# Optimization experiments

Measured on AMD Instinct MI355X. Metric: run time of the kernel, lower is better.

The kernel has to match this reference:

```python
import jax, jax.numpy as jnp
import numpy as np

D = 192          # d_model = d_perc = d_tech
H = 3            # n_heads
HD = D // H      # head_dim = 64
FP = 128         # fingerprint_dim
EPS_LN = 1e-5


def _layernorm(x, g, b):
    mu = jnp.mean(x, axis=-1, keepdims=True)
    var = jnp.var(x, axis=-1, keepdims=True)
    return (x - mu) * jax.lax.rsqrt(var + EPS_LN) * g + b


def setup_inputs() -> dict:
    key = jax.random.key(0)
    ks = jax.random.split(key, 32)
    B = 65536
    s = 0.05
    inp = {
        'perc_vec': jax.random.normal(ks[0], (B, D), jnp.float32),
        'tech_vec': jax.random.normal(ks[1], (B, D), jnp.float32),
        # proj_p / proj_t (torch Linear: [out, in])
        'Wp': jax.random.normal(ks[2], (D, D), jnp.float32) * s,
        'bp': jax.random.normal(ks[3], (D,), jnp.float32) * s,
        'Wt': jax.random.normal(ks[4], (D, D), jnp.float32) * s,
        'bt': jax.random.normal(ks[5], (D,), jnp.float32) * s,
        # MultiheadAttention packed in-proj [3D, D] and out-proj [D, D]
        'in_w': jax.random.normal(ks[6], (3 * D, D), jnp.float32) * s,
        'in_b': jax.random.normal(ks[7], (3 * D,), jnp.float32) * s,
        'out_w': jax.random.normal(ks[8], (D, D), jnp.float32) * s,
        'out_b': jax.random.normal(ks[9], (D,), jnp.float32) * s,
        # FFN
        'ffn_w1': jax.random.normal(ks[10], (2 * D, D), jnp.float32) * s,
        'ffn_b1': jax.random.normal(ks[11], (2 * D,), jnp.float32) * s,
        'ffn_w2': jax.random.normal(ks[12], (D, 2 * D), jnp.float32) * s,
        'ffn_b2': jax.random.normal(ks[13], (D,), jnp.float32) * s,
        # LayerNorms
        'ln1_g': jnp.ones((D,), jnp.float32),
        'ln1_b': jnp.zeros((D,), jnp.float32),
        'ln2_g': jnp.ones((D,), jnp.float32),
        'ln2_b': jnp.zeros((D,), jnp.float32),
        # classifier head
        'cls_w1': jax.random.normal(ks[14], (D, D), jnp.float32) * s,
        'cls_b1': jax.random.normal(ks[15], (D,), jnp.float32) * s,
        'cls_w2': jax.random.normal(ks[16], (3, D), jnp.float32) * s,
        'cls_b2': jax.random.normal(ks[17], (3,), jnp.float32) * s,
        # fingerprint head
        'fp_w': jax.random.normal(ks[18], (FP, D), jnp.float32) * s,
        'fp_b': jax.random.normal(ks[19], (FP,), jnp.float32) * s,
    }
    return inp


def reference(perc_vec, tech_vec, Wp, bp, Wt, bt, in_w, in_b, out_w, out_b,
              ffn_w1, ffn_b1, ffn_w2, ffn_b2, ln1_g, ln1_b, ln2_g, ln2_b,
              cls_w1, cls_b1, cls_w2, cls_b2, fp_w, fp_b):
    B = perc_vec.shape[0]
    # projections -> 2-token sequence [B, 2, D]
    p = perc_vec @ Wp.T + bp
    t = tech_vec @ Wt.T + bt
    seq = jnp.stack([p, t], axis=1)

    # self-attention (eval mode, no dropout)
    qkv = seq @ in_w.T + in_b                     # [B, 2, 3D]
    q, k, v = jnp.split(qkv, 3, axis=-1)
    q = q.reshape(B, 2, H, HD).transpose(0, 2, 1, 3)  # [B, H, 2, HD]
    k = k.reshape(B, 2, H, HD).transpose(0, 2, 1, 3)
    v = v.reshape(B, 2, H, HD).transpose(0, 2, 1, 3)
    scores = jnp.einsum('bhqd,bhkd->bhqk', q, k) / np.sqrt(HD).astype(np.float32)
    attn = jax.nn.softmax(scores, axis=-1)
    ctx = jnp.einsum('bhqk,bhkd->bhqd', attn, v)      # [B, H, 2, HD]
    ctx = ctx.transpose(0, 2, 1, 3).reshape(B, 2, D)
    attn_out = ctx @ out_w.T + out_b

    x = _layernorm(seq + attn_out, ln1_g, ln1_b)
    h = jax.nn.relu(x @ ffn_w1.T + ffn_b1)
    ffn = h @ ffn_w2.T + ffn_b2
    x = _layernorm(x + ffn, ln2_g, ln2_b)

    z = x.mean(axis=1)                                # [B, D]
    logits = jax.nn.relu(z @ cls_w1.T + cls_b1) @ cls_w2.T + cls_b2  # [B, 3]
    probs = jax.nn.sigmoid(logits)
    fp = z @ fp_w.T + fp_b
    fp = fp / jnp.maximum(jnp.linalg.norm(fp, axis=-1, keepdims=True), 1e-12)
    # (presence_p, decode_reliability, artifact_risk, fingerprint)
    return probs[:, 0:1], probs[:, 1:2], probs[:, 2:3], fp
```

## Files before the change

### kernel.cpp

```cpp
#include <hip/hip_runtime.h>
#include <hip/hip_bf16.h>
#include <math.h>

#define D 192
#define RPB 16
typedef unsigned short u16;
typedef __attribute__((ext_vector_type(8))) short short8;
typedef __attribute__((ext_vector_type(4))) float float4v;

__device__ __forceinline__ float b2f(u16 u){ union{unsigned i; float f;}c; c.i=(unsigned)u<<16; return c.f; }
__device__ __forceinline__ u16  f2b(float f){
    union{float f; unsigned i;}c; c.f=f;
    unsigned r = c.i + 0x7FFFu + ((c.i>>16)&1u);
    return (u16)(r>>16);
}
__device__ __forceinline__ float sel4(float a0,float a1,float a2,float a3,int s){
    return s==0?a0:(s==1?a1:(s==2?a2:a3));
}

#define WP_OFF   0
#define WT_OFF   36864
#define INW_OFF  73728
#define OUTW_OFF 184320
#define FW1_OFF  221184
#define FW2_OFF  294912
#define CW1_OFF  368640
#define FPW_OFF  405504
#define W_TOTAL  430080

__global__ __launch_bounds__(256)
void cvt_weights(const float* __restrict__ Wp, const float* __restrict__ Wt,
                 const float* __restrict__ in_w, const float* __restrict__ out_w,
                 const float* __restrict__ fw1, const float* __restrict__ fw2,
                 const float* __restrict__ cw1, const float* __restrict__ fpw,
                 u16* __restrict__ ws)
{
    int idx = blockIdx.x * 256 + threadIdx.x;
    if (idx >= W_TOTAL) return;
    const float* src; int off; int K = 192;
    if      (idx < WT_OFF)   { src = Wp;   off = WP_OFF; }
    else if (idx < INW_OFF)  { src = Wt;   off = WT_OFF; }
    else if (idx < OUTW_OFF) { src = in_w; off = INW_OFF; }
    else if (idx < FW1_OFF)  { src = out_w;off = OUTW_OFF; }
    else if (idx < FW2_OFF)  { src = fw1;  off = FW1_OFF; }
    else if (idx < CW1_OFF)  { src = fw2;  off = FW2_OFF; K = 384; }
    else if (idx < FPW_OFF)  { src = cw1;  off = CW1_OFF; }
    else                     { src = fpw;  off = FPW_OFF; }
    int lin = idx - off;
    int n = lin / K, k = lin - n*K;
    int swz = ((n>>4)*(K>>5) + (k>>5))*512 + ((n&15)<<5) + (k&31);
    ws[off + swz] = f2b(src[lin]);
}

template<int KT, int MT>
__device__ __forceinline__ void load_afrags(short8 (&A)[MT][KT], const u16* base,
                                            int stride, int lane16, int quad)
{
    #pragma unroll
    for (int mt = 0; mt < MT; ++mt)
        #pragma unroll
        for (int ks = 0; ks < KT; ++ks)
            A[mt][ks] = *(const short8*)(base + (mt*16 + lane16)*stride + ks*32 + quad*8);
}

template<int KT, int MT, int NTW>
__device__ __forceinline__ void run_gemm(const short8 (&A)[MT][KT],
    const u16* __restrict__ wsb, const float* __restrict__ bias,
    u16* dst, float* dstf, int dstride,
    const u16* resid, int rstride, bool relu, int rmul, int roff,
    int wave, int lane16, int quad)
{
    #pragma unroll
    for (int i = 0; i < NTW; ++i) {
        int nt = wave + 4*i, n0 = nt*16;
        float4v c[MT];
        #pragma unroll
        for (int mt = 0; mt < MT; ++mt) c[mt] = (float4v){0.f,0.f,0.f,0.f};
        #pragma unroll
        for (int ks = 0; ks < KT; ++ks) {
            short8 b = *(const short8*)(wsb + (size_t)((nt*KT + ks)<<9) + (lane16<<5) + (quad<<3));
            #pragma unroll
            for (int mt = 0; mt < MT; ++mt)
                c[mt] = __builtin_amdgcn_mfma_f32_16x16x32_bf16(A[mt][ks], b, c[mt], 0,0,0);
        }
        float bv = bias[n0 + lane16];
        #pragma unroll
        for (int mt = 0; mt < MT; ++mt)
            #pragma unroll
            for (int ii = 0; ii < 4; ++ii) {
                int dr = (mt*16 + quad*4 + ii)*rmul + roff;
                float v = c[mt][ii] + bv;
                if (resid) v += b2f(resid[dr*rstride + n0 + lane16]);
                if (relu)  v = fmaxf(v, 0.f);
                if (dst) dst [dr*dstride + n0 + lane16] = f2b(v);
                else     dstf[dr*dstride + n0 + lane16] = v;
            }
    }
}

#define S1 200
#define SH 392
#define A_INP 0
#define A_INT 3200
#define A_SEQ 6400
#define A_CTX 0
#define A_X1  6400
#define A_H   0
#define A_Z   0
#define A_CH  3200
#define A_FPF 6400
#define ARENA_U16 12800

__global__ __launch_bounds__(256, 4)
void fusion_mfma_kernel(
    const float* __restrict__ perc, const float* __restrict__ tech,
    const float* __restrict__ bp,   const float* __restrict__ bt,
    const float* __restrict__ in_b, const float* __restrict__ out_b,
    const float* __restrict__ fb1,  const float* __restrict__ fb2,
    const float* __restrict__ ln1g, const float* __restrict__ ln1b,
    const float* __restrict__ ln2g, const float* __restrict__ ln2b,
    const float* __restrict__ cb1,  const float* __restrict__ cw2,
    const float* __restrict__ cb2,  const float* __restrict__ fpb,
    const u16*   __restrict__ ws,
    float* __restrict__ out, int B)
{
    __shared__ __align__(16) u16 arena[ARENA_U16];
    __shared__ __align__(16) float satt[16][3][4];
    __shared__ float wavered[4][32][2];
    __shared__ float smu[32], srs[32], srn[16];

    const int tid = threadIdx.x;
    const int wave = tid >> 6, lane = tid & 63;
    const int lane16 = lane & 15, quad = lane >> 4;
    const int row0 = blockIdx.x * RPB;
    float* fpf = (float*)(arena + A_FPF);

    #pragma unroll
    for (int it = 0; it < 3; ++it) {
        int idx = it*256 + tid;
        int arr = idx >= 384 ? 1 : 0;
        int rem = arr ? idx - 384 : idx;
        int r = rem / 24, g = rem - r*24;
        const float* src = arr ? tech : perc;
        const float4* s4 = (const float4*)(src + (size_t)(row0 + r)*D + g*8);
        float4 lo = s4[0], hi = s4[1];
        short8 o;
        o[0]=(short)f2b(lo.x); o[1]=(short)f2b(lo.y); o[2]=(short)f2b(lo.z); o[3]=(short)f2b(lo.w);
        o[4]=(short)f2b(hi.x); o[5]=(short)f2b(hi.y); o[6]=(short)f2b(hi.z); o[7]=(short)f2b(hi.w);
        *(short8*)(arena + (arr ? A_INT : A_INP) + r*S1 + g*8) = o;
    }
    __syncthreads();

    {
        short8 A1[1][6];
        load_afrags<6,1>(A1, arena + A_INP, S1, lane16, quad);
        run_gemm<6,1,3>(A1, ws + WP_OFF, bp, arena + A_SEQ, nullptr, S1,
                        nullptr, 0, false, 2, 0, wave, lane16, quad);
        load_afrags<6,1>(A1, arena + A_INT, S1, lane16, quad);
        run_gemm<6,1,3>(A1, ws + WT_OFF, bt, arena + A_SEQ, nullptr, S1,
                        nullptr, 0, false, 2, 1, wave, lane16, quad);
    }
    __syncthreads();

    short8 A2[2][6];
    load_afrags<6,2>(A2, arena + A_SEQ, S1, lane16, quad);
    {
        float* satt_w = (float*)arena;
        #pragma unroll
        for (int i = 0; i < 3; ++i) {
            int nt = wave + 4*i;
            float4v ck[2] = {(float4v){0,0,0,0},(float4v){0,0,0,0}};
            #pragma unroll
            for (int ks = 0; ks < 6; ++ks) {
                short8 b = *(const short8*)(ws + INW_OFF + 192*192 + ((nt*6+ks)<<9) + (lane16<<5) + (quad<<3));
                ck[0] = __builtin_amdgcn_mfma_f32_16x16x32_bf16(A2[0][ks], b, ck[0], 0,0,0);
                ck[1] = __builtin_amdgcn_mfma_f32_16x16x32_bf16(A2[1][ks], b, ck[1], 0,0,0);
            }
            float bvk = in_b[192 + nt*16 + lane16];
            float4v cq[2] = {(float4v){0,0,0,0},(float4v){0,0,0,0}};
            #pragma unroll
            for (int ks = 0; ks < 6; ++ks) {
                short8 b = *(const short8*)(ws + INW_OFF + ((nt*6+ks)<<9) + (lane16<<5) + (quad<<3));
                cq[0] = __builtin_amdgcn_mfma_f32_16x16x32_bf16(A2[0][ks], b, cq[0], 0,0,0);
                cq[1] = __builtin_amdgcn_mfma_f32_16x16x32_bf16(A2[1][ks], b, cq[1], 0,0,0);
            }
            float bvq = in_b[nt*16 + lane16];
            float sc[2][2][4];
            #pragma unroll
            for (int mt = 0; mt < 2; ++mt)
                #pragma unroll
                for (int p = 0; p < 2; ++p) {
                    float q0 = cq[mt][2*p] + bvq, q1 = cq[mt][2*p+1] + bvq;
                    float k0 = ck[mt][2*p] + bvk, k1 = ck[mt][2*p+1] + bvk;
                    sc[mt][p][0] = q0*k0; sc[mt][p][1] = q0*k1;
                    sc[mt][p][2] = q1*k0; sc[mt][p][3] = q1*k1;
                }
            #pragma unroll
            for (int mt = 0; mt < 2; ++mt)
                #pragma unroll
                for (int p = 0; p < 2; ++p)
                    #pragma unroll
                    for (int c = 0; c < 4; ++c) {
                        float v = sc[mt][p][c];
                        v += __shfl_xor(v, 1); v += __shfl_xor(v, 2);
                        v += __shfl_xor(v, 4); v += __shfl_xor(v, 8);
                        sc[mt][p][c] = v;
                    }
            if ((lane16 >> 2) == i) {
                int c = lane16 & 3;
                #pragma unroll
                for (int mt = 0; mt < 2; ++mt)
                    #pragma unroll
                    for (int p = 0; p < 2; ++p) {
                        float vv = sel4(sc[mt][p][0], sc[mt][p][1], sc[mt][p][2], sc[mt][p][3], c);
                        satt_w[(wave*16 + (2*quad + p + 8*mt))*12 + i*4 + c] = vv;
                    }
            }
        }
    }
    __syncthreads();

    if (tid < 96) {
        const float* satt_w = (const float*)arena;
        int r = tid / 6, rem = tid - r*6;
        int h = rem >> 1, qt = rem & 1;
        float s0 = 0.f, s1 = 0.f;
        #pragma unroll
        for (int w = 0; w < 4; ++w) {
            s0 += satt_w[(w*16 + r)*12 + h*4 + qt*2 + 0];
            s1 += satt_w[(w*16 + r)*12 + h*4 + qt*2 + 1];
        }
        s0 *= 0.125f; s1 *= 0.125f;
        float m = fmaxf(s0, s1);
        float e0 = expf(s0 - m), e1 = expf(s1 - m);
        float inv = 1.f / (e0 + e1);
        satt[r][h][qt*2 + 0] = e0 * inv;
        satt[r][h][qt*2 + 1] = e1 * inv;
    }
    __syncthreads();

    #pragma unroll
    for (int i = 0; i < 3; ++i) {
        int nt = wave + 4*i, col = nt*16 + lane16;
        float4v cv[2] = {(float4v){0,0,0,0},(float4v){0,0,0,0}};
        #pragma unroll
        for (int ks = 0; ks < 6; ++ks) {
            short8 b = *(const short8*)(ws + INW_OFF + 384*192 + ((nt*6+ks)<<9) + (lane16<<5) + (quad<<3));
            cv[0] = __builtin_amdgcn_mfma_f32_16x16x32_bf16(A2[0][ks], b, cv[0], 0,0,0);
            cv[1] = __builtin_amdgcn_mfma_f32_16x16x32_bf16(A2[1][ks], b, cv[1], 0,0,0);
        }
        float bv = in_b[384 + col];
        #pragma unroll
        for (int mt = 0; mt < 2; ++mt)
            #pragma unroll
            for (int p = 0; p < 2; ++p) {
                float v0 = cv[mt][2*p] + bv, v1 = cv[mt][2*p+1] + bv;
                int r = 2*quad + p + 8*mt;
                float4 pa = *(const float4*)&satt[r][i][0];
                arena[A_CTX + (2*r    )*S1 + col] = f2b(pa.x*v0 + pa.y*v1);
                arena[A_CTX + (2*r + 1)*S1 + col] = f2b(pa.z*v0 + pa.w*v1);
            }
    }
    __syncthreads();

    float4v x1r[3][2];
    {
        short8 Ac[2][6];
        load_afrags<6,2>(Ac, arena + A_CTX, S1, lane16, quad);
        #pragma unroll
        for (int i = 0; i < 3; ++i) {
            int nt = wave + 4*i, col = nt*16 + lane16;
            x1r[i][0] = (float4v){0,0,0,0}; x1r[i][1] = (float4v){0,0,0,0};
            #pragma unroll
            for (int ks = 0; ks < 6; ++ks) {
                short8 b = *(const short8*)(ws + OUTW_OFF + ((nt*6+ks)<<9) + (lane16<<5) + (quad<<3));
                x1r[i][0] = __builtin_amdgcn_mfma_f32_16x16x32_bf16(Ac[0][ks], b, x1r[i][0], 0,0,0);
                x1r[i][1] = __builtin_amdgcn_mfma_f32_16x16x32_bf16(Ac[1][ks], b, x1r[i][1], 0,0,0);
            }
            float bv = out_b[col];
            #pragma unroll
            for (int mt = 0; mt < 2; ++mt)
                #pragma unroll
                for (int ii = 0; ii < 4; ++ii) {
                    int row = quad*4 + ii + 16*mt;
                    x1r[i][mt][ii] += bv + b2f(arena[A_SEQ + row*S1 + col]);
                }
        }
        float sr[2][4], s2r[2][4];
        #pragma unroll
        for (int mt = 0; mt < 2; ++mt)
            #pragma unroll
            for (int ii = 0; ii < 4; ++ii) {
                float a0 = x1r[0][mt][ii], a1 = x1r[1][mt][ii], a2 = x1r[2][mt][ii];
                float s = a0 + a1 + a2;
                float s2 = a0*a0 + a1*a1 + a2*a2;
                s  += __shfl_xor(s, 1);  s  += __shfl_xor(s, 2);
                s  += __shfl_xor(s, 4);  s  += __shfl_xor(s, 8);
                s2 += __shfl_xor(s2, 1); s2 += __shfl_xor(s2, 2);
                s2 += __shfl_xor(s2, 4); s2 += __shfl_xor(s2, 8);
                sr[mt][ii] = s; s2r[mt][ii] = s2;
            }
        int l = lane16;
        float rowlo = sel4(sr[0][0], sr[0][1], sr[0][2], sr[0][3], l & 3);
        float rowhi = sel4(sr[1][0], sr[1][1], sr[1][2], sr[1][3], l & 3);
        float row2lo = sel4(s2r[0][0], s2r[0][1], s2r[0][2], s2r[0][3], l & 3);
        float row2hi = sel4(s2r[1][0], s2r[1][1], s2r[1][2], s2r[1][3], l & 3);
        float sv = (l & 4) ? rowhi : rowlo;
        float s2v = (l & 4) ? row2hi : row2lo;
        float val = (l & 8) ? s2v : sv;
        wavered[wave][quad*4 + (l & 3) + 16*((l >> 2) & 1)][l >> 3] = val;
    }
    __syncthreads();
    if (tid < 32) {
        float s = 0.f, s2 = 0.f;
        #pragma unroll
        for (int w = 0; w < 4; ++w) { s += wavered[w][tid][0]; s2 += wavered[w][tid][1]; }
        float mu = s * (1.f/192.f);
        float var = s2 * (1.f/192.f) - mu*mu;
        smu[tid] = mu; srs[tid] = rsqrtf(var + 1e-5f);
    }
    __syncthreads();

    #pragma unroll
    for (int i = 0; i < 3; ++i) {
        int col = (wave + 4*i)*16 + lane16;
        float g = ln1g[col], bb = ln1b[col];
        #pragma unroll
        for (int mt = 0; mt < 2; ++mt)
            #pragma unroll
            for (int ii = 0; ii < 4; ++ii) {
                int row = quad*4 + ii + 16*mt;
                float x = (x1r[i][mt][ii] - smu[row]) * srs[row] * g + bb;
                x1r[i][mt][ii] = x;
                arena[A_X1 + row*S1 + col] = f2b(x);
            }
    }
    __syncthreads();

    {
        short8 Ax[2][6];
        load_afrags<6,2>(Ax, arena + A_X1, S1, lane16, quad);
        __syncthreads();
        run_gemm<6,2,6>(Ax, ws + FW1_OFF, fb1, arena + A_H, nullptr, SH,
                        nullptr, 0, true, 1, 0, wave, lane16, quad);
    }
    __syncthreads();

    {
        float4v c2[3][2];
        #pragma unroll
        for (int i = 0; i < 3; ++i) { c2[i][0] = (float4v){0,0,0,0}; c2[i][1] = (float4v){0,0,0,0}; }
        #pragma unroll
        for (int kc = 0; kc < 2; ++kc) {
            short8 Af[2][6];
            load_afrags<6,2>(Af, arena + A_H + kc*192, SH, lane16, quad);
            #pragma unroll
            for (int i = 0; i < 3; ++i) {
                int nt = wave + 4*i;
                #pragma unroll
                for (int ks = 0; ks < 6; ++ks) {
                    short8 b = *(const short8*)(ws + FW2_OFF + ((nt*12 + kc*6 + ks)<<9) + (lane16<<5) + (quad<<3));
                    c2[i][0] = __builtin_amdgcn_mfma_f32_16x16x32_bf16(Af[0][ks], b, c2[i][0], 0,0,0);
                    c2[i][1] = __builtin_amdgcn_mfma_f32_16x16x32_bf16(Af[1][ks], b, c2[i][1], 0,0,0);
                }
            }
        }
        #pragma unroll
        for (int i = 0; i < 3; ++i) {
            float bv = fb2[(wave + 4*i)*16 + lane16];
            #pragma unroll
            for (int mt = 0; mt < 2; ++mt)
                #pragma unroll
                for (int ii = 0; ii < 4; ++ii)
                    c2[i][mt][ii] += bv + x1r[i][mt][ii];
        }
        float sr[2][4], s2r[2][4];
        #pragma unroll
        for (int mt = 0; mt < 2; ++mt)
            #pragma unroll
            for (int ii = 0; ii < 4; ++ii) {
                float a0 = c2[0][mt][ii], a1 = c2[1][mt][ii], a2 = c2[2][mt][ii];
                float s = a0 + a1 + a2;
                float s2 = a0*a0 + a1*a1 + a2*a2;
                s  += __shfl_xor(s, 1);  s  += __shfl_xor(s, 2);
                s  += __shfl_xor(s, 4);  s  += __shfl_xor(s, 8);
                s2 += __shfl_xor(s2, 1); s2 += __shfl_xor(s2, 2);
                s2 += __shfl_xor(s2, 4); s2 += __shfl_xor(s2, 8);
                sr[mt][ii] = s; s2r[mt][ii] = s2;
            }
        int l = lane16;
        float rowlo = sel4(sr[0][0], sr[0][1], sr[0][2], sr[0][3], l & 3);
        float rowhi = sel4(sr[1][0], sr[1][1], sr[1][2], sr[1][3], l & 3);
        float row2lo = sel4(s2r[0][0], s2r[0][1], s2r[0][2], s2r[0][3], l & 3);
        float row2hi = sel4(s2r[1][0], s2r[1][1], s2r[1][2], s2r[1][3], l & 3);
        float sv = (l & 4) ? rowhi : rowlo;
        float s2v = (l & 4) ? row2hi : row2lo;
        float val = (l & 8) ? s2v : sv;
        wavered[wave][quad*4 + (l & 3) + 16*((l >> 2) & 1)][l >> 3] = val;
        __syncthreads();
        if (tid < 32) {
            float s = 0.f, s2 = 0.f;
            #pragma unroll
            for (int w = 0; w < 4; ++w) { s += wavered[w][tid][0]; s2 += wavered[w][tid][1]; }
            float mu = s * (1.f/192.f);
            float var = s2 * (1.f/192.f) - mu*mu;
            smu[tid] = mu; srs[tid] = rsqrtf(var + 1e-5f);
        }
        __syncthreads();
        #pragma unroll
        for (int i = 0; i < 3; ++i) {
            int col = (wave + 4*i)*16 + lane16;
            float g = ln2g[col], bb = ln2b[col];
            #pragma unroll
            for (int mt = 0; mt < 2; ++mt)
                #pragma unroll
                for (int p = 0; p < 2; ++p) {
                    int r = 2*quad + p + 8*mt;
                    float n0v = (c2[i][mt][2*p]   - smu[2*r  ]) * srs[2*r  ] * g + bb;
                    float n1v = (c2[i][mt][2*p+1] - smu[2*r+1]) * srs[2*r+1] * g + bb;
                    arena[A_Z + r*S1 + col] = f2b(0.5f*(n0v + n1v));
                }
        }
    }
    __syncthreads();

    {
        short8 A1[1][6];
        load_afrags<6,1>(A1, arena + A_Z, S1, lane16, quad);
        run_gemm<6,1,3>(A1, ws + CW1_OFF, cb1, arena + A_CH, nullptr, S1,
                        nullptr, 0, true, 1, 0, wave, lane16, quad);
        run_gemm<6,1,2>(A1, ws + FPW_OFF, fpb, nullptr, fpf, 128,
                        nullptr, 0, false, 1, 0, wave, lane16, quad);
    }
    __syncthreads();

    if (tid < 192) {
        int g4 = tid >> 2, sub = tid & 3;
        int r = g4 / 3, cc = g4 - r*3;
        const float* w = cw2 + (size_t)cc * D + sub*48;
        const u16* hr = arena + A_CH + r*S1 + sub*48;
        float a = 0.f;
        #pragma unroll
        for (int i = 0; i < 6; ++i) {
            short8 hv = *(const short8*)(hr + i*8);
            float4 w0 = ((const float4*)w)[2*i], w1 = ((const float4*)w)[2*i+1];
            float wv[8] = {w0.x,w0.y,w0.z,w0.w,w1.x,w1.y,w1.z,w1.w};
            #pragma unroll
            for (int j = 0; j < 8; ++j) a += wv[j] * b2f((u16)hv[j]);
        }
        a += __shfl_xor(a, 1); a += __shfl_xor(a, 2);
        if (sub == 0) {
            a += cb2[cc];
            out[(size_t)cc * B + (size_t)(row0 + r)] = 1.f / (1.f + expf(-a));
        }
    } else {
        int t = tid - 192;
        int r = t >> 2, sub = t & 3;
        const float4* fp4 = (const float4*)(fpf + r*128 + sub*32);
        float s2 = 0.f;
        #pragma unroll
        for (int i = 0; i < 8; ++i) {
            float4 v = fp4[i];
            s2 += v.x*v.x + v.y*v.y + v.z*v.z + v.w*v.w;
        }
        s2 += __shfl_xor(s2, 1); s2 += __shfl_xor(s2, 2);
        if (sub == 0) srn[r] = 1.f / fmaxf(sqrtf(s2), 1e-12f);
    }
    __syncthreads();

    #pragma unroll
    for (int it = 0; it < 2; ++it) {
        int idx = it*256 + tid;
        int r = idx >> 5, c = idx & 31;
        float4 v = ((const float4*)(fpf + r*128))[c];
        float sc = srn[r];
        float4 o; o.x = v.x*sc; o.y = v.y*sc; o.z = v.z*sc; o.w = v.w*sc;
        ((float4*)(out + (size_t)3*B + (size_t)(row0 + r)*128))[c] = o;
    }
}

extern "C" void kernel_launch(void* const* d_in, const int* in_sizes, int n_in,
                              void* d_out, int out_size, void* d_ws, size_t ws_size,
                              hipStream_t stream) {
    if (ws_size < (size_t)W_TOTAL * 2) return;

    const float* perc = (const float*)d_in[0];
    const float* tech = (const float*)d_in[1];
    const float* Wp   = (const float*)d_in[2];
    const float* bp   = (const float*)d_in[3];
    const float* Wt   = (const float*)d_in[4];
    const float* bt   = (const float*)d_in[5];
    const float* in_w = (const float*)d_in[6];
    const float* in_b = (const float*)d_in[7];
    const float* ow   = (const float*)d_in[8];
    const float* ob   = (const float*)d_in[9];
    const float* fw1  = (const float*)d_in[10];
    const float* fb1  = (const float*)d_in[11];
    const float* fw2  = (const float*)d_in[12];
    const float* fb2  = (const float*)d_in[13];
    const float* ln1g = (const float*)d_in[14];
    const float* ln1b = (const float*)d_in[15];
    const float* ln2g = (const float*)d_in[16];
    const float* ln2b = (const float*)d_in[17];
    const float* cw1  = (const float*)d_in[18];
    const float* cb1  = (const float*)d_in[19];
    const float* cw2  = (const float*)d_in[20];
    const float* cb2  = (const float*)d_in[21];
    const float* fpw  = (const float*)d_in[22];
    const float* fpb  = (const float*)d_in[23];

    u16* ws = (u16*)d_ws;
    int B = in_sizes[0] / D;

    hipLaunchKernelGGL(cvt_weights, dim3((W_TOTAL + 255)/256), dim3(256), 0, stream,
                       Wp, Wt, in_w, ow, fw1, fw2, cw1, fpw, ws);

    hipLaunchKernelGGL(fusion_mfma_kernel, dim3(B / RPB), dim3(256), 0, stream,
                       perc, tech, bp, bt, in_b, ob, fb1, fb2,
                       ln1g, ln1b, ln2g, ln2b, cb1, cw2, cb2, fpb,
                       ws, (float*)d_out, B);
}
```

Baseline: 421.7 us.

## Keep LN1 output in LDS instead of registers across FFN to cut VGPRs

The post-attention residual is now written to LDS as bf16 while its row sums are accumulated on the fly, and LayerNorm1 runs as a vectorized in-place pass over LDS. The FFN2 residual is read back from LDS, so the 24-float x1r array no longer stays live across the FFN GEMMs. This lowers register pressure and drops one barrier. In exchange the arena grows (ARENA_U16 from 12800 to 18944), which adds LDS traffic and could limit occupancy. The residual is also rounded to bf16 before LN2, which costs some precision.

```diff
diff --git a/kernel.cpp b/kernel.cpp
--- a/kernel.cpp
+++ b/kernel.cpp
@@ -100,16 +100,16 @@
 
 #define S1 200
 #define SH 392
-#define A_INP 0
-#define A_INT 3200
-#define A_SEQ 6400
+#define A_STG_P 0
+#define A_STG_T 3200
+#define A_SEQ 12544
 #define A_CTX 0
-#define A_X1  6400
+#define A_X1  12544
 #define A_H   0
 #define A_Z   0
 #define A_CH  3200
 #define A_FPF 6400
-#define ARENA_U16 12800
+#define ARENA_U16 18944
 
 __global__ __launch_bounds__(256, 4)
 void fusion_mfma_kernel(
@@ -147,16 +147,16 @@
         short8 o;
         o[0]=(short)f2b(lo.x); o[1]=(short)f2b(lo.y); o[2]=(short)f2b(lo.z); o[3]=(short)f2b(lo.w);
         o[4]=(short)f2b(hi.x); o[5]=(short)f2b(hi.y); o[6]=(short)f2b(hi.z); o[7]=(short)f2b(hi.w);
-        *(short8*)(arena + (arr ? A_INT : A_INP) + r*S1 + g*8) = o;
+        *(short8*)(arena + (arr ? A_STG_T : A_STG_P) + r*S1 + g*8) = o;
     }
     __syncthreads();
 
     {
         short8 A1[1][6];
-        load_afrags<6,1>(A1, arena + A_INP, S1, lane16, quad);
+        load_afrags<6,1>(A1, arena + A_STG_P, S1, lane16, quad);
         run_gemm<6,1,3>(A1, ws + WP_OFF, bp, arena + A_SEQ, nullptr, S1,
                         nullptr, 0, false, 2, 0, wave, lane16, quad);
-        load_afrags<6,1>(A1, arena + A_INT, S1, lane16, quad);
+        load_afrags<6,1>(A1, arena + A_STG_T, S1, lane16, quad);
         run_gemm<6,1,3>(A1, ws + WT_OFF, bt, arena + A_SEQ, nullptr, S1,
                         nullptr, 0, false, 2, 1, wave, lane16, quad);
     }
@@ -263,19 +263,23 @@
     }
     __syncthreads();
 
-    float4v x1r[3][2];
     {
         short8 Ac[2][6];
         load_afrags<6,2>(Ac, arena + A_CTX, S1, lane16, quad);
+        float sa[2][4], s2a[2][4];
+        #pragma unroll
+        for (int mt = 0; mt < 2; ++mt)
+            #pragma unroll
+            for (int ii = 0; ii < 4; ++ii) { sa[mt][ii] = 0.f; s2a[mt][ii] = 0.f; }
         #pragma unroll
         for (int i = 0; i < 3; ++i) {
             int nt = wave + 4*i, col = nt*16 + lane16;
-            x1r[i][0] = (float4v){0,0,0,0}; x1r[i][1] = (float4v){0,0,0,0};
+            float4v c[2] = {(float4v){0,0,0,0},(float4v){0,0,0,0}};
             #pragma unroll
             for (int ks = 0; ks < 6; ++ks) {
                 short8 b = *(const short8*)(ws + OUTW_OFF + ((nt*6+ks)<<9) + (lane16<<5) + (quad<<3));
-                x1r[i][0] = __builtin_amdgcn_mfma_f32_16x16x32_bf16(Ac[0][ks], b, x1r[i][0], 0,0,0);
-                x1r[i][1] = __builtin_amdgcn_mfma_f32_16x16x32_bf16(Ac[1][ks], b, x1r[i][1], 0,0,0);
+                c[0] = __builtin_amdgcn_mfma_f32_16x16x32_bf16(Ac[0][ks], b, c[0], 0,0,0);
+                c[1] = __builtin_amdgcn_mfma_f32_16x16x32_bf16(Ac[1][ks], b, c[1], 0,0,0);
             }
             float bv = out_b[col];
             #pragma unroll
@@ -283,28 +287,27 @@
                 #pragma unroll
                 for (int ii = 0; ii < 4; ++ii) {
                     int row = quad*4 + ii + 16*mt;
-                    x1r[i][mt][ii] += bv + b2f(arena[A_SEQ + row*S1 + col]);
+                    float v = c[mt][ii] + bv + b2f(arena[A_SEQ + row*S1 + col]);
+                    arena[A_X1 + row*S1 + col] = f2b(v);
+                    sa[mt][ii] += v; s2a[mt][ii] += v*v;
                 }
         }
-        float sr[2][4], s2r[2][4];
         #pragma unroll
         for (int mt = 0; mt < 2; ++mt)
             #pragma unroll
             for (int ii = 0; ii < 4; ++ii) {
-                float a0 = x1r[0][mt][ii], a1 = x1r[1][mt][ii], a2 = x1r[2][mt][ii];
-                float s = a0 + a1 + a2;
-                float s2 = a0*a0 + a1*a1 + a2*a2;
+                float s = sa[mt][ii], s2 = s2a[mt][ii];
                 s  += __shfl_xor(s, 1);  s  += __shfl_xor(s, 2);
                 s  += __shfl_xor(s, 4);  s  += __shfl_xor(s, 8);
                 s2 += __shfl_xor(s2, 1); s2 += __shfl_xor(s2, 2);
                 s2 += __shfl_xor(s2, 4); s2 += __shfl_xor(s2, 8);
-                sr[mt][ii] = s; s2r[mt][ii] = s2;
+                sa[mt][ii] = s; s2a[mt][ii] = s2;
             }
         int l = lane16;
-        float rowlo = sel4(sr[0][0], sr[0][1], sr[0][2], sr[0][3], l & 3);
-        float rowhi = sel4(sr[1][0], sr[1][1], sr[1][2], sr[1][3], l & 3);
-        float row2lo = sel4(s2r[0][0], s2r[0][1], s2r[0][2], s2r[0][3], l & 3);
-        float row2hi = sel4(s2r[1][0], s2r[1][1], s2r[1][2], s2r[1][3], l & 3);
+        float rowlo = sel4(sa[0][0], sa[0][1], sa[0][2], sa[0][3], l & 3);
+        float rowhi = sel4(sa[1][0], sa[1][1], sa[1][2], sa[1][3], l & 3);
+        float row2lo = sel4(s2a[0][0], s2a[0][1], s2a[0][2], s2a[0][3], l & 3);
+        float row2hi = sel4(s2a[1][0], s2a[1][1], s2a[1][2], s2a[1][3], l & 3);
         float sv = (l & 4) ? rowhi : rowlo;
         float s2v = (l & 4) ? row2hi : row2lo;
         float val = (l & 8) ? s2v : sv;
@@ -322,25 +325,27 @@
     __syncthreads();
 
     #pragma unroll
-    for (int i = 0; i < 3; ++i) {
-        int col = (wave + 4*i)*16 + lane16;
-        float g = ln1g[col], bb = ln1b[col];
-        #pragma unroll
-        for (int mt = 0; mt < 2; ++mt)
-            #pragma unroll
-            for (int ii = 0; ii < 4; ++ii) {
-                int row = quad*4 + ii + 16*mt;
-                float x = (x1r[i][mt][ii] - smu[row]) * srs[row] * g + bb;
-                x1r[i][mt][ii] = x;
-                arena[A_X1 + row*S1 + col] = f2b(x);
-            }
+    for (int it = 0; it < 3; ++it) {
+        int idx = it*256 + tid;
+        int tok = idx / 24, g = idx - tok*24;
+        float mu = smu[tok], rs = srs[tok];
+        float4 ga = ((const float4*)(ln1g + g*8))[0], gb = ((const float4*)(ln1g + g*8))[1];
+        float4 ba = ((const float4*)(ln1b + g*8))[0], bb = ((const float4*)(ln1b + g*8))[1];
+        float gg[8]  = {ga.x,ga.y,ga.z,ga.w,gb.x,gb.y,gb.z,gb.w};
+        float bbv[8] = {ba.x,ba.y,ba.z,ba.w,bb.x,bb.y,bb.z,bb.w};
+        u16* p = arena + A_X1 + tok*S1 + g*8;
+        short8 v = *(const short8*)p;
+        short8 o;
+        #pragma unroll
+        for (int j = 0; j < 8; ++j)
+            o[j] = (short)f2b((b2f((u16)v[j]) - mu)*rs*gg[j] + bbv[j]);
+        *(short8*)p = o;
     }
     __syncthreads();
 
     {
         short8 Ax[2][6];
         load_afrags<6,2>(Ax, arena + A_X1, S1, lane16, quad);
-        __syncthreads();
         run_gemm<6,2,6>(Ax, ws + FW1_OFF, fb1, arena + A_H, nullptr, SH,
                         nullptr, 0, true, 1, 0, wave, lane16, quad);
     }
@@ -367,14 +372,17 @@
         }
         #pragma unroll
         for (int i = 0; i < 3; ++i) {
-            float bv = fb2[(wave + 4*i)*16 + lane16];
+            int col = (wave + 4*i)*16 + lane16;
+            float bv = fb2[col];
             #pragma unroll
             for (int mt = 0; mt < 2; ++mt)
                 #pragma unroll
-                for (int ii = 0; ii < 4; ++ii)
-                    c2[i][mt][ii] += bv + x1r[i][mt][ii];
-        }
-        float sr[2][4], s2r[2][4];
+                for (int ii = 0; ii < 4; ++ii) {
+                    int row = quad*4 + ii + 16*mt;
+                    c2[i][mt][ii] += bv + b2f(arena[A_X1 + row*S1 + col]);
+                }
+        }
+        float sa[2][4], s2a[2][4];
         #pragma unroll
         for (int mt = 0; mt < 2; ++mt)
             #pragma unroll
@@ -386,13 +394,13 @@
                 s  += __shfl_xor(s, 4);  s  += __shfl_xor(s, 8);
                 s2 += __shfl_xor(s2, 1); s2 += __shfl_xor(s2, 2);
                 s2 += __shfl_xor(s2, 4); s2 += __shfl_xor(s2, 8);
-                sr[mt][ii] = s; s2r[mt][ii] = s2;
+                sa[mt][ii] = s; s2a[mt][ii] = s2;
             }
         int l = lane16;
-        float rowlo = sel4(sr[0][0], sr[0][1], sr[0][2], sr[0][3], l & 3);
-        float rowhi = sel4(sr[1][0], sr[1][1], sr[1][2], sr[1][3], l & 3);
-        float row2lo = sel4(s2r[0][0], s2r[0][1], s2r[0][2], s2r[0][3], l & 3);
-        float row2hi = sel4(s2r[1][0], s2r[1][1], s2r[1][2], s2r[1][3], l & 3);
+        float rowlo = sel4(sa[0][0], sa[0][1], sa[0][2], sa[0][3], l & 3);
+        float rowhi = sel4(sa[1][0], sa[1][1], sa[1][2], sa[1][3], l & 3);
+        float row2lo = sel4(s2a[0][0], s2a[0][1], s2a[0][2], s2a[0][3], l & 3);
+        float row2hi = sel4(s2a[1][0], s2a[1][1], s2a[1][2], s2a[1][3], l & 3);
         float sv = (l & 4) ? rowhi : rowlo;
         float s2v = (l & 4) ? row2hi : row2lo;
         float val = (l & 8) ? s2v : sv;
```

Result: faster. 401.3 us (-4.9%).
